# Kernel tuning notes

Measured on AMD Instinct MI355X. Metric: run time of the kernel, lower is better.

## Reference

```python
import jax, jax.numpy as jnp
import numpy as np

K = 2            # number of kernel experts (1 common + 1 learned)
TEMPERATURE = 31.0
STRIDE = (2, 2)
KSIZE = 5


def setup_inputs() -> dict:
    key = jax.random.key(0)
    ks = jax.random.split(key, 7)
    B, Cin, H, W = 128, 96, 63, 63
    Cout = 256
    x = jax.random.normal(ks[0], (B, Cin, H, W), jnp.float32)
    common_weight = jax.random.normal(ks[1], (1, Cout, Cin, KSIZE, KSIZE), jnp.float32) * 0.05
    common_bias = jax.random.normal(ks[2], (1, Cout), jnp.float32) * 0.01
    expert_weight = jax.random.normal(ks[3], (1, Cout, Cin, KSIZE, KSIZE), jnp.float32) * 0.05
    expert_bias = jax.random.normal(ks[4], (1, Cout), jnp.float32) * 0.01
    att_w1 = jax.random.normal(ks[5], (24, Cin), jnp.float32) * 0.1   # fc1: 1x1 conv == linear
    att_w2 = jax.random.normal(ks[6], (K, 24), jnp.float32) * 0.1     # fc2
    return {"x": x, "common_weight": common_weight, "common_bias": common_bias,
            "expert_weight": expert_weight, "expert_bias": expert_bias,
            "att_w1": att_w1, "att_w2": att_w2}


def reference(x, common_weight, common_bias, expert_weight, expert_bias, att_w1, att_w2):
    B, Cin, H, W = x.shape
    Cout = common_weight.shape[1]

    # attention2d: global average pool -> fc1 -> relu -> fc2 -> softmax(logits / T)
    pooled = jnp.mean(x, axis=(2, 3))                       # [B, Cin]
    hidden = jax.nn.relu(pooled @ att_w1.T)                 # [B, 24]
    logits = hidden @ att_w2.T                              # [B, K]
    att = jax.nn.softmax(logits / TEMPERATURE, axis=1)      # [B, K]

    # aggregate per-sample kernels: [B,K] @ [K, Cout*Cin*k*k]
    weight = jnp.concatenate([common_weight, expert_weight], axis=0).reshape(K, -1)
    agg_w = (att @ weight).reshape(B * Cout, Cin, KSIZE, KSIZE)
    bias2 = jnp.concatenate([common_bias, expert_bias], axis=0)  # [K, Cout]
    agg_b = (att @ bias2).reshape(-1)                            # [B*Cout]

    # grouped conv with groups = batch_size (per-sample conv)
    xg = x.reshape(1, B * Cin, H, W)
    out = jax.lax.conv_general_dilated(
        xg, agg_w, window_strides=STRIDE, padding='VALID',
        feature_group_count=B,
        dimension_numbers=('NCHW', 'OIHW', 'NCHW'))             # [1, B*Cout, Ho, Wo]
    out = out + agg_b[None, :, None, None]
    Ho, Wo = out.shape[2], out.shape[3]
    return out.reshape(B, Cout, Ho, Wo)
```

## Files before the change

### kernel.cpp

```cpp
#include <hip/hip_runtime.h>
#include <math.h>

#define CIN   96
#define HW_IN 3969
#define WIN   63
#define COUT  256
#define NPIX  900
#define WO    30
#define KTOT  2400
#define NB    128
#define KSTEPS 75
#define AGG_OFF 65536
#define AGG_BYTES ((size_t)NB * KSTEPS * 16384)

typedef short bf16x8 __attribute__((ext_vector_type(8)));
typedef float f32x4  __attribute__((ext_vector_type(4)));
typedef __attribute__((address_space(1))) const void gas_t;
typedef __attribute__((address_space(3))) void las_t;

__device__ __forceinline__ unsigned pk2(float lo, float hi) {
  unsigned r;
  asm("v_cvt_pk_bf16_f32 %0, %1, %2" : "=v"(r) : "v"(lo), "v"(hi));
  return r;
}

__global__ __launch_bounds__(256) void pool_kernel(const float* __restrict__ x,
                                                   float* __restrict__ pooled) {
  const int ci = blockIdx.x;
  const int b  = blockIdx.y;
  const float* xc = x + ((size_t)b * CIN + ci) * HW_IN;
  const int tid = threadIdx.x, lane = tid & 63, wv = tid >> 6;
  float s = 0.f;
  const int head = (4 - (ci & 3)) & 3;
  if (tid < head) s += xc[tid];
  const float4* x4 = (const float4*)(xc + head);
  const int n4 = (HW_IN - head) >> 2;
  for (int i = tid; i < n4; i += 256) { float4 v = x4[i]; s += (v.x + v.y) + (v.z + v.w); }
  const int done = head + (n4 << 2);
  if (tid < HW_IN - done) s += xc[done + tid];
  #pragma unroll
  for (int off = 32; off > 0; off >>= 1) s += __shfl_xor(s, off, 64);
  __shared__ float part[4];
  if (lane == 0) part[wv] = s;
  __syncthreads();
  if (tid == 0)
    pooled[(size_t)b * CIN + ci] = (part[0] + part[1] + part[2] + part[3]) * (1.0f / HW_IN);
}

__global__ __launch_bounds__(64) void attn_kernel(const float* __restrict__ pooled,
                                                  const float* __restrict__ w1,
                                                  const float* __restrict__ w2,
                                                  float* __restrict__ att) {
  const int b = blockIdx.x;
  const int tid = threadIdx.x;
  __shared__ float hidden[24];
  const float* pb = pooled + (size_t)b * CIN;
  if (tid < 24) {
    float h = 0.f;
    const float* w1r = w1 + tid * CIN;
    for (int ci = 0; ci < CIN; ++ci) h += pb[ci] * w1r[ci];
    hidden[tid] = fmaxf(h, 0.f);
  }
  __syncthreads();
  if (tid == 0) {
    float l0 = 0.f, l1 = 0.f;
    for (int j = 0; j < 24; ++j) { l0 += hidden[j] * w2[j]; l1 += hidden[j] * w2[24 + j]; }
    l0 *= (1.0f / 31.0f); l1 *= (1.0f / 31.0f);
    const float m = fmaxf(l0, l1);
    const float e0 = expf(l0 - m), e1 = expf(l1 - m);
    const float inv = 1.0f / (e0 + e1);
    att[b * 2 + 0] = e0 * inv;
    att[b * 2 + 1] = e1 * inv;
  }
}

__global__ __launch_bounds__(256) void agg_kernel(const float* __restrict__ wc,
                                                  const float* __restrict__ we,
                                                  const float* __restrict__ att,
                                                  unsigned* __restrict__ aggW) {
  const int ks = blockIdx.x;
  const int t  = blockIdx.y;
  const int b  = blockIdx.z;
  const float a0 = att[b * 2 + 0];
  const float a1 = att[b * 2 + 1];
  unsigned* dst = aggW + (((size_t)b * KSTEPS + ks) << 12) + (t << 11);
  #pragma unroll
  for (int uu = 0; uu < 2; ++uu) {
    const int u = threadIdx.x + uu * 256;
    const int row = u >> 2, slot = u & 3;
    const int oct = slot ^ ((row >> 1) & 3);
    const float* pc = wc + (size_t)(t * 128 + row) * KTOT + ks * 32 + oct * 8;
    const float* pe = we + (size_t)(t * 128 + row) * KTOT + ks * 32 + oct * 8;
    float4 c0 = ((const float4*)pc)[0], c1 = ((const float4*)pc)[1];
    float4 e0 = ((const float4*)pe)[0], e1 = ((const float4*)pe)[1];
    uint4 q;
    q.x = pk2(a0 * c0.x + a1 * e0.x, a0 * c0.y + a1 * e0.y);
    q.y = pk2(a0 * c0.z + a1 * e0.z, a0 * c0.w + a1 * e0.w);
    q.z = pk2(a0 * c1.x + a1 * e1.x, a0 * c1.y + a1 * e1.y);
    q.w = pk2(a0 * c1.z + a1 * e1.z, a0 * c1.w + a1 * e1.w);
    ((uint4*)dst)[u] = q;
  }
}

__global__ __launch_bounds__(512) void conv_pre(
    const float* __restrict__ x,
    const float* __restrict__ bc, const float* __restrict__ be,
    const float* __restrict__ att, const unsigned* __restrict__ aggW,
    float* __restrict__ out) {
  const int flat = (int)(blockIdx.x + (blockIdx.z << 3));
  const int wg   = ((flat & 7) << 7) | (flat >> 3);
  const int p0 = (wg & 7) * 128;
  const int b  = wg >> 3;

  __shared__ short As[2][256 * 32];
  __shared__ short Bs[2][128 * 32];
  __shared__ int   koffAll[KTOT];
  __shared__ float biasS[COUT];

  const int tid  = threadIdx.x;
  const int wv   = tid >> 6, lane = tid & 63;
  const int quad = lane >> 4, lm = lane & 15;
  const int wm = (wv >> 1) * 64;
  const int wn = (wv & 1) * 64;

  if (tid < COUT) {
    const float a0 = att[b * 2 + 0], a1 = att[b * 2 + 1];
    biasS[tid] = a0 * bc[tid] + a1 * be[tid];
  }
  for (int k = tid; k < KTOT; k += 512) {
    const int ci = k / 25, r = k - ci * 25;
    const int kh = r / 5,  kw = r - kh * 5;
    koffAll[k] = ci * HW_IN + kh * WIN + kw;
  }

  const int rowT = tid >> 2;
  const int oct  = (tid & 3) * 8;
  const int bu   = (tid & 3) ^ ((rowT >> 1) & 3);

  const float* xb = x + (size_t)b * (CIN * HW_IN);
  const int pA = p0 + rowT;
  const int ohA = pA / WO, owA = pA - ohA * WO;
  const bool vA = pA < NPIX;
  const float* xpA = xb + (ohA * 2) * WIN + owA * 2;

  const char* aggB = (const char*)aggW
                   + ((size_t)b * KSTEPS << 14)
                   + (((wv << 7) + lane) << 4);
  const int xoct = quad ^ ((lm >> 1) & 3);

  const f32x4 zero = {0.f, 0.f, 0.f, 0.f};
  f32x4 acc[4][4];
  #pragma unroll
  for (int i = 0; i < 4; ++i)
    #pragma unroll
    for (int j = 0; j < 4; ++j) acc[i][j] = zero;

  __syncthreads();

  {
    __builtin_amdgcn_global_load_lds((gas_t*)aggB, (las_t*)&As[0][wv << 10], 16, 0, 0);
    __builtin_amdgcn_global_load_lds((gas_t*)(aggB + 1024), (las_t*)&As[0][(wv << 10) + 512], 16, 0, 0);
    const int4 ka = *(const int4*)&koffAll[oct];
    const int4 kb = *(const int4*)&koffAll[oct + 4];
    uint4 qa = {0u, 0u, 0u, 0u};
    if (vA) {
      qa.x = pk2(xpA[ka.x], xpA[ka.y]); qa.y = pk2(xpA[ka.z], xpA[ka.w]);
      qa.z = pk2(xpA[kb.x], xpA[kb.y]); qa.w = pk2(xpA[kb.z], xpA[kb.w]);
    }
    *(uint4*)&Bs[0][rowT * 32 + bu * 8] = qa;
  }
  __syncthreads();

  for (int ks = 0; ks < KSTEPS - 1; ++ks) {
    const int cur = ks & 1, nxt = cur ^ 1;
    const char* src = aggB + ((size_t)(ks + 1) << 14);
    __builtin_amdgcn_global_load_lds((gas_t*)src, (las_t*)&As[nxt][wv << 10], 16, 0, 0);
    __builtin_amdgcn_global_load_lds((gas_t*)(src + 1024), (las_t*)&As[nxt][(wv << 10) + 512], 16, 0, 0);
    const int k1 = (ks + 1) << 5;
    const int4 ka = *(const int4*)&koffAll[k1 + oct];
    const int4 kb = *(const int4*)&koffAll[k1 + oct + 4];
    float g0 = 0.f, g1 = 0.f, g2 = 0.f, g3 = 0.f, g4 = 0.f, g5 = 0.f, g6 = 0.f, g7 = 0.f;
    if (vA) {
      g0 = xpA[ka.x]; g1 = xpA[ka.y]; g2 = xpA[ka.z]; g3 = xpA[ka.w];
      g4 = xpA[kb.x]; g5 = xpA[kb.y]; g6 = xpA[kb.z]; g7 = xpA[kb.w];
    }
    bf16x8 af[4], bfv[4];
    #pragma unroll
    for (int i = 0; i < 4; ++i)
      af[i] = *(const bf16x8*)&As[cur][(wm + i * 16 + lm) * 32 + xoct * 8];
    #pragma unroll
    for (int j = 0; j < 4; ++j)
      bfv[j] = *(const bf16x8*)&Bs[cur][(wn + j * 16 + lm) * 32 + xoct * 8];
    #pragma unroll
    for (int i = 0; i < 4; ++i)
      #pragma unroll
      for (int j = 0; j < 4; ++j)
        acc[i][j] = __builtin_amdgcn_mfma_f32_16x16x32_bf16(af[i], bfv[j], acc[i][j], 0, 0, 0);
    uint4 qa;
    qa.x = pk2(g0, g1); qa.y = pk2(g2, g3); qa.z = pk2(g4, g5); qa.w = pk2(g6, g7);
    *(uint4*)&Bs[nxt][rowT * 32 + bu * 8] = qa;
    __syncthreads();
  }

  {
    const int cur = (KSTEPS - 1) & 1;
    bf16x8 af[4], bfv[4];
    #pragma unroll
    for (int i = 0; i < 4; ++i)
      af[i] = *(const bf16x8*)&As[cur][(wm + i * 16 + lm) * 32 + xoct * 8];
    #pragma unroll
    for (int j = 0; j < 4; ++j)
      bfv[j] = *(const bf16x8*)&Bs[cur][(wn + j * 16 + lm) * 32 + xoct * 8];
    #pragma unroll
    for (int i = 0; i < 4; ++i)
      #pragma unroll
      for (int j = 0; j < 4; ++j)
        acc[i][j] = __builtin_amdgcn_mfma_f32_16x16x32_bf16(af[i], bfv[j], acc[i][j], 0, 0, 0);
  }

  float* outb = out + (size_t)b * COUT * NPIX;
  #pragma unroll
  for (int j = 0; j < 4; ++j) {
    const int p = p0 + wn + j * 16 + lm;
    if (p < NPIX) {
      #pragma unroll
      for (int i = 0; i < 4; ++i) {
        #pragma unroll
        for (int r = 0; r < 4; ++r) {
          const int m = wm + i * 16 + quad * 4 + r;
          outb[(size_t)m * NPIX + p] = acc[i][j][r] + biasS[m];
        }
      }
    }
  }
}

__global__ __launch_bounds__(256) void conv_fb(
    const float* __restrict__ x,
    const float* __restrict__ wc, const float* __restrict__ we,
    const float* __restrict__ bc, const float* __restrict__ be,
    const float* __restrict__ att, float* __restrict__ out) {
  const int flat = (int)(blockIdx.x + (blockIdx.y << 3) + (blockIdx.z << 4));
  const int wg   = ((flat & 7) << 8) | (flat >> 3);
  const int p0 = (wg & 7) * 128;
  const int m0 = ((wg >> 3) & 1) * 128;
  const int b  = wg >> 4;

  __shared__ short As[128 * 40];
  __shared__ short Bs[128][40];
  __shared__ int   koffAll[KTOT];
  __shared__ float biasS[128];

  const int tid  = threadIdx.x;
  const int wv   = tid >> 6, lane = tid & 63;
  const int quad = lane >> 4, lm = lane & 15;
  const int wm = (wv >> 1) * 64;
  const int wn = (wv & 1) * 64;

  const float a0 = att[b * 2 + 0];
  const float a1 = att[b * 2 + 1];

  if (tid < 128) biasS[tid] = a0 * bc[m0 + tid] + a1 * be[m0 + tid];
  for (int k = tid; k < KTOT; k += 256) {
    const int ci = k / 25, r = k - ci * 25;
    const int kh = r / 5,  kw = r - kh * 5;
    koffAll[k] = ci * HW_IN + kh * WIN + kw;
  }

  const int rowT = tid >> 2;
  const int oct  = (tid & 3) * 8;

  const float* xb = x + (size_t)b * (CIN * HW_IN);
  const int pA = p0 + rowT, pB = p0 + rowT + 64;
  const int ohA = pA / WO, owA = pA - ohA * WO;
  const int ohB = pB / WO, owB = pB - ohB * WO;
  const bool vA = pA < NPIX, vB = pB < NPIX;
  const float* xpA = xb + (ohA * 2) * WIN + owA * 2;
  const float* xpB = xb + (ohB * 2) * WIN + owB * 2;

  const float* wcr0 = wc + (size_t)(m0 + rowT) * KTOT + oct;
  const float* wer0 = we + (size_t)(m0 + rowT) * KTOT + oct;

  const f32x4 zero = {0.f, 0.f, 0.f, 0.f};
  f32x4 acc[4][4];
  #pragma unroll
  for (int i = 0; i < 4; ++i)
    #pragma unroll
    for (int j = 0; j < 4; ++j) acc[i][j] = zero;

  for (int k0 = 0; k0 < KTOT; k0 += 32) {
    __syncthreads();
    #pragma unroll
    for (int t = 0; t < 2; ++t) {
      const float4* pc = (const float4*)(wcr0 + (size_t)t * 64 * KTOT + k0);
      const float4* pe = (const float4*)(wer0 + (size_t)t * 64 * KTOT + k0);
      float4 c0 = pc[0], c1 = pc[1];
      float4 e0 = pe[0], e1 = pe[1];
      uint4 q;
      q.x = pk2(a0 * c0.x + a1 * e0.x, a0 * c0.y + a1 * e0.y);
      q.y = pk2(a0 * c0.z + a1 * e0.z, a0 * c0.w + a1 * e0.w);
      q.z = pk2(a0 * c1.x + a1 * e1.x, a0 * c1.y + a1 * e1.y);
      q.w = pk2(a0 * c1.z + a1 * e1.z, a0 * c1.w + a1 * e1.w);
      *(uint4*)&As[(rowT + t * 64) * 40 + oct] = q;
    }
    const int4 ka = *(const int4*)&koffAll[k0 + oct];
    const int4 kb = *(const int4*)&koffAll[k0 + oct + 4];
    {
      uint4 q = {0u, 0u, 0u, 0u};
      if (vA) {
        q.x = pk2(xpA[ka.x], xpA[ka.y]); q.y = pk2(xpA[ka.z], xpA[ka.w]);
        q.z = pk2(xpA[kb.x], xpA[kb.y]); q.w = pk2(xpA[kb.z], xpA[kb.w]);
      }
      *(uint4*)&Bs[rowT][oct] = q;
    }
    {
      uint4 q = {0u, 0u, 0u, 0u};
      if (vB) {
        q.x = pk2(xpB[ka.x], xpB[ka.y]); q.y = pk2(xpB[ka.z], xpB[ka.w]);
        q.z = pk2(xpB[kb.x], xpB[kb.y]); q.w = pk2(xpB[kb.z], xpB[kb.w]);
      }
      *(uint4*)&Bs[rowT + 64][oct] = q;
    }
    __syncthreads();
    bf16x8 af[4], bfv[4];
    #pragma unroll
    for (int i = 0; i < 4; ++i) af[i]  = *(const bf16x8*)&As[(wm + i * 16 + lm) * 40 + quad * 8];
    #pragma unroll
    for (int j = 0; j < 4; ++j) bfv[j] = *(const bf16x8*)&Bs[wn + j * 16 + lm][quad * 8];
    #pragma unroll
    for (int i = 0; i < 4; ++i)
      #pragma unroll
      for (int j = 0; j < 4; ++j)
        acc[i][j] = __builtin_amdgcn_mfma_f32_16x16x32_bf16(af[i], bfv[j], acc[i][j], 0, 0, 0);
  }

  float* outb = out + ((size_t)b * COUT + m0) * NPIX;
  #pragma unroll
  for (int j = 0; j < 4; ++j) {
    const int p = p0 + wn + j * 16 + lm;
    if (p < NPIX) {
      #pragma unroll
      for (int i = 0; i < 4; ++i) {
        #pragma unroll
        for (int r = 0; r < 4; ++r) {
          const int m = wm + i * 16 + quad * 4 + r;
          outb[(size_t)m * NPIX + p] = acc[i][j][r] + biasS[m];
        }
      }
    }
  }
}

extern "C" void kernel_launch(void* const* d_in, const int* in_sizes, int n_in,
                              void* d_out, int out_size, void* d_ws, size_t ws_size,
                              hipStream_t stream) {
  (void)in_sizes; (void)n_in; (void)out_size;
  const float* x  = (const float*)d_in[0];
  const float* wc = (const float*)d_in[1];
  const float* bc = (const float*)d_in[2];
  const float* we = (const float*)d_in[3];
  const float* be = (const float*)d_in[4];
  const float* w1 = (const float*)d_in[5];
  const float* w2 = (const float*)d_in[6];
  float* out = (float*)d_out;

  float* att    = (float*)d_ws;
  float* pooled = att + 256;
  unsigned* aggW = (unsigned*)((char*)d_ws + AGG_OFF);

  pool_kernel<<<dim3(CIN, NB), 256, 0, stream>>>(x, pooled);
  attn_kernel<<<NB, 64, 0, stream>>>(pooled, w1, w2, att);

  if (ws_size >= AGG_OFF + AGG_BYTES) {
    agg_kernel<<<dim3(KSTEPS, 2, NB), 256, 0, stream>>>(wc, we, att, aggW);
    conv_pre<<<dim3(8, 1, NB), 512, 0, stream>>>(x, bc, be, att, aggW, out);
  } else {
    conv_fb<<<dim3(8, 2, NB), 256, 0, stream>>>(x, wc, we, bc, be, att, out);
  }
}
```

Before: 598.6 us.

## Fuse attention MLP into weight aggregation kernel and reuse weight loads across samples

Removes the separate attention kernel launch by computing each sample's hidden layer and softmax inside the aggregation kernel, redundantly per block. Each block now loads a slice of the common and expert weights once and reuses it in registers for 8 samples, which cuts repeated global reads of the weights. The attention values are still written out once (by the ks==0 blocks) for the conv kernel. The cost is duplicated small MLP work in every block and fewer, larger blocks.

```diff
diff --git a/kernel.cpp b/kernel.cpp
--- a/kernel.cpp
+++ b/kernel.cpp
@@ -74,31 +74,72 @@
   }
 }
 
-__global__ __launch_bounds__(256) void agg_kernel(const float* __restrict__ wc,
+__global__ __launch_bounds__(512) void agg_kernel(const float* __restrict__ wc,
                                                   const float* __restrict__ we,
-                                                  const float* __restrict__ att,
+                                                  const float* __restrict__ pooled,
+                                                  const float* __restrict__ w1,
+                                                  const float* __restrict__ w2,
+                                                  float* __restrict__ att,
                                                   unsigned* __restrict__ aggW) {
   const int ks = blockIdx.x;
-  const int t  = blockIdx.y;
-  const int b  = blockIdx.z;
-  const float a0 = att[b * 2 + 0];
-  const float a1 = att[b * 2 + 1];
-  unsigned* dst = aggW + (((size_t)b * KSTEPS + ks) << 12) + (t << 11);
-  #pragma unroll
-  for (int uu = 0; uu < 2; ++uu) {
-    const int u = threadIdx.x + uu * 256;
-    const int row = u >> 2, slot = u & 3;
-    const int oct = slot ^ ((row >> 1) & 3);
-    const float* pc = wc + (size_t)(t * 128 + row) * KTOT + ks * 32 + oct * 8;
-    const float* pe = we + (size_t)(t * 128 + row) * KTOT + ks * 32 + oct * 8;
-    float4 c0 = ((const float4*)pc)[0], c1 = ((const float4*)pc)[1];
-    float4 e0 = ((const float4*)pe)[0], e1 = ((const float4*)pe)[1];
-    uint4 q;
-    q.x = pk2(a0 * c0.x + a1 * e0.x, a0 * c0.y + a1 * e0.y);
-    q.y = pk2(a0 * c0.z + a1 * e0.z, a0 * c0.w + a1 * e0.w);
-    q.z = pk2(a0 * c1.x + a1 * e1.x, a0 * c1.y + a1 * e1.y);
-    q.w = pk2(a0 * c1.z + a1 * e1.z, a0 * c1.w + a1 * e1.w);
-    ((uint4*)dst)[u] = q;
+  const int b0 = blockIdx.y * 8;
+  const int tid = threadIdx.x;
+
+  __shared__ float hidS[8][25];
+  __shared__ float attS[8][2];
+
+  if (tid < 192) {
+    const int bb = tid / 24, j = tid - bb * 24;
+    const float* pb  = pooled + (size_t)(b0 + bb) * CIN;
+    const float* w1r = w1 + j * CIN;
+    float h = 0.f;
+    for (int ci = 0; ci < CIN; ++ci) h += pb[ci] * w1r[ci];
+    hidS[bb][j] = fmaxf(h, 0.f);
+  }
+
+  const int row0 = tid >> 2, slot = tid & 3;
+  const int oct  = slot ^ ((row0 >> 1) & 3);
+  const float* pc0 = wc + (size_t)row0 * KTOT + ks * 32 + oct * 8;
+  const float* pe0 = we + (size_t)row0 * KTOT + ks * 32 + oct * 8;
+  const float* pc1 = pc0 + (size_t)128 * KTOT;
+  const float* pe1 = pe0 + (size_t)128 * KTOT;
+  const float4 c00 = ((const float4*)pc0)[0], c01 = ((const float4*)pc0)[1];
+  const float4 e00 = ((const float4*)pe0)[0], e01 = ((const float4*)pe0)[1];
+  const float4 c10 = ((const float4*)pc1)[0], c11 = ((const float4*)pc1)[1];
+  const float4 e10 = ((const float4*)pe1)[0], e11 = ((const float4*)pe1)[1];
+
+  __syncthreads();
+  if (tid < 8) {
+    float l0 = 0.f, l1 = 0.f;
+    for (int j = 0; j < 24; ++j) { l0 += hidS[tid][j] * w2[j]; l1 += hidS[tid][j] * w2[24 + j]; }
+    l0 *= (1.0f / 31.0f); l1 *= (1.0f / 31.0f);
+    const float m = fmaxf(l0, l1);
+    const float e0 = expf(l0 - m), e1 = expf(l1 - m);
+    const float inv = 1.0f / (e0 + e1);
+    attS[tid][0] = e0 * inv;
+    attS[tid][1] = e1 * inv;
+    if (ks == 0) {
+      att[(b0 + tid) * 2 + 0] = attS[tid][0];
+      att[(b0 + tid) * 2 + 1] = attS[tid][1];
+    }
+  }
+  __syncthreads();
+
+  #pragma unroll 2
+  for (int bb = 0; bb < 8; ++bb) {
+    const float a0 = attS[bb][0], a1 = attS[bb][1];
+    uint4 q0, q1;
+    q0.x = pk2(a0 * c00.x + a1 * e00.x, a0 * c00.y + a1 * e00.y);
+    q0.y = pk2(a0 * c00.z + a1 * e00.z, a0 * c00.w + a1 * e00.w);
+    q0.z = pk2(a0 * c01.x + a1 * e01.x, a0 * c01.y + a1 * e01.y);
+    q0.w = pk2(a0 * c01.z + a1 * e01.z, a0 * c01.w + a1 * e01.w);
+    q1.x = pk2(a0 * c10.x + a1 * e10.x, a0 * c10.y + a1 * e10.y);
+    q1.y = pk2(a0 * c10.z + a1 * e10.z, a0 * c10.w + a1 * e10.w);
+    q1.z = pk2(a0 * c11.x + a1 * e11.x, a0 * c11.y + a1 * e11.y);
+    q1.w = pk2(a0 * c11.z + a1 * e11.z, a0 * c11.w + a1 * e11.w);
+    unsigned* dst = aggW + (((size_t)(b0 + bb) * KSTEPS + ks) << 12);
+    ((uint4*)dst)[tid]       = q0;
+    ((uint4*)dst)[tid + 512] = q1;
   }
 }
 
@@ -369,12 +410,12 @@
   unsigned* aggW = (unsigned*)((char*)d_ws + AGG_OFF);
 
   pool_kernel<<<dim3(CIN, NB), 256, 0, stream>>>(x, pooled);
-  attn_kernel<<<NB, 64, 0, stream>>>(pooled, w1, w2, att);
 
   if (ws_size >= AGG_OFF + AGG_BYTES) {
-    agg_kernel<<<dim3(KSTEPS, 2, NB), 256, 0, stream>>>(wc, we, att, aggW);
+    agg_kernel<<<dim3(KSTEPS, 16), 512, 0, stream>>>(wc, we, pooled, w1, w2, att, aggW);
     conv_pre<<<dim3(8, 1, NB), 512, 0, stream>>>(x, bc, be, att, aggW, out);
   } else {
+    attn_kernel<<<NB, 64, 0, stream>>>(pooled, w1, w2, att);
     conv_fb<<<dim3(8, 2, NB), 256, 0, stream>>>(x, wc, we, bc, be, att, out);
   }
 }
```

New measurement: 599.7 us. About the same (+0.2%).
